# Kernel tuning notes

Measured on AMD Instinct MI355X. Metric: run time of the kernel, lower is better.

The kernel has to match this reference:

```python
import jax, jax.numpy as jnp
import numpy as np
from jax import lax

K = 3; KK = K * K; S = 1; P = 1; D = 1
BN_EPS = 1e-5


def setup_inputs() -> dict:
    key = jax.random.key(0)
    ks = jax.random.split(key, 4)
    B, C, H, W = 8, 128, 64, 64
    cout = 128
    # xavier-ish scales for conv weights
    def xavier(k, shape):
        fan_in = shape[1] * shape[2] * shape[3]
        fan_out = shape[0] * shape[2] * shape[3]
        limit = np.sqrt(6.0 / (fan_in + fan_out))
        return jax.random.uniform(k, shape, jnp.float32, -limit, limit)
    return {
        "x": jax.random.normal(ks[0], (B, C, H, W), jnp.float32),
        "w_off": xavier(ks[1], (2 * KK, C, K, K)),
        "b_off": jnp.zeros((2 * KK,), jnp.float32),
        "w_mod": xavier(ks[2], (KK, C, K, K)),
        "b_mod": jnp.zeros((KK,), jnp.float32),
        "w_reg": xavier(ks[3], (cout, C, K, K)),
        "b_reg": jnp.zeros((cout,), jnp.float32),
        "gamma": jnp.ones((cout,), jnp.float32),
        "beta": jnp.zeros((cout,), jnp.float32),
    }


def _conv(x, w, b):
    y = lax.conv_general_dilated(x, w, (S, S), [(P, P), (P, P)],
                                 rhs_dilation=(D, D),
                                 dimension_numbers=("NCHW", "OIHW", "NCHW"))
    return y + b[None, :, None, None]


def _deform_conv(x, offset, mask, w_reg, b_reg):
    B, C, H, W = x.shape
    Ho, Wo = offset.shape[2], offset.shape[3]
    # torchvision layout: [B, 2*KK, Ho, Wo], interleaved (dy, dx) per tap
    off = offset.reshape(B, KK, 2, Ho, Wo)
    dy, dx = off[:, :, 0], off[:, :, 1]                      # [B,KK,Ho,Wo]
    ki = jnp.arange(KK) // K
    kj = jnp.arange(KK) % K
    base_y = (jnp.arange(Ho) * S - P)[None, :, None] + (ki * D)[:, None, None]  # [KK,Ho,1]
    base_x = (jnp.arange(Wo) * S - P)[None, None, :] + (kj * D)[:, None, None]  # [KK,1,Wo]
    py = base_y[None].astype(x.dtype) + dy                   # [B,KK,Ho,Wo]
    px = base_x[None].astype(x.dtype) + dx

    y0f = jnp.floor(py); x0f = jnp.floor(px)
    ly = py - y0f; lx = px - x0f
    y0 = y0f.astype(jnp.int32); x0 = x0f.astype(jnp.int32)
    y1 = y0 + 1; x1 = x0 + 1

    def gather(iy, ix):
        valid = ((iy >= 0) & (iy < H) & (ix >= 0) & (ix < W)).astype(x.dtype)
        iyc = jnp.clip(iy, 0, H - 1)
        ixc = jnp.clip(ix, 0, W - 1)
        v = jax.vmap(lambda img, a, b: img[:, a, b])(x, iyc, ixc)  # [B,C,KK,Ho,Wo]
        return v * valid[:, None]

    val = (gather(y0, x0) * ((1 - ly) * (1 - lx))[:, None]
           + gather(y0, x1) * ((1 - ly) * lx)[:, None]
           + gather(y1, x0) * (ly * (1 - lx))[:, None]
           + gather(y1, x1) * (ly * lx)[:, None])               # [B,C,KK,Ho,Wo]

    patches = val * mask[:, None]                               # modulated samples
    wr = w_reg.reshape(w_reg.shape[0], C, KK)
    out = jnp.einsum("ock,bckhw->bohw", wr, patches)
    return out + b_reg[None, :, None, None]


def reference(x, w_off, b_off, w_mod, b_mod, w_reg, b_reg, gamma, beta):
    offset = _conv(x, w_off, b_off)
    modulator = 2.0 * jax.nn.sigmoid(_conv(x, w_mod, b_mod))
    y = _deform_conv(x, offset, modulator, w_reg, b_reg)
    # BatchNorm2d (training-mode batch statistics) + ReLU
    mu = y.mean(axis=(0, 2, 3), keepdims=True)
    var = y.var(axis=(0, 2, 3), keepdims=True)
    y = (y - mu) * lax.rsqrt(var + BN_EPS)
    y = y * gamma[None, :, None, None] + beta[None, :, None, None]
    return jax.nn.relu(y)
```

## Files before the change

kernel.cpp:

```cpp
#include <hip/hip_runtime.h>
#include <math.h>

#define H 64
#define W 64
#define C 128
#define NB 8
#define COUT 128
#define HWi 4096
#define NKC 36
#define PADu 40

typedef __attribute__((ext_vector_type(8))) short short8;
typedef __attribute__((ext_vector_type(8))) unsigned short ushort8;
typedef __attribute__((ext_vector_type(4))) unsigned int uint4v;
typedef __attribute__((ext_vector_type(4))) float f32x4;

__device__ __forceinline__ unsigned short f2bf(float f){
    unsigned u = __float_as_uint(f);
    unsigned r = (u + 0x7FFFu + ((u >> 16) & 1u)) >> 16;
    return (unsigned short)r;
}
__device__ __forceinline__ float bf2f(unsigned short u){
    return __uint_as_float(((unsigned)u) << 16);
}
__device__ __forceinline__ unsigned cvtpk_bf16(float lo, float hi){
    unsigned r;
    asm("v_cvt_pk_bf16_f32 %0, %1, %2" : "=v"(r) : "v"(lo), "v"(hi));
    return r;
}

__global__ void k_pre(const float* __restrict__ x, unsigned short* __restrict__ xTp,
                      const float* __restrict__ w_reg, const float* __restrict__ w_off,
                      const float* __restrict__ w_mod, const float* __restrict__ b_off,
                      const float* __restrict__ b_mod,
                      unsigned short* __restrict__ wAv, unsigned short* __restrict__ w27A,
                      float* __restrict__ biasom, float* __restrict__ psum){
    int tid = threadIdx.x;
    if (blockIdx.x >= 528){
        int i = (blockIdx.x - 528) * 256 + tid;
        if (i < 147456){
            int kc = i >> 12, rem = i & 4095;
            int q = rem >> 10, r = (rem >> 3) & 127, j = rem & 7;
            int kk = kc * 32 + q * 8 + j, k = kk >> 7, c = kk & 127;
            wAv[i] = f2bf(w_reg[r * 1152 + c * 9 + k]);
        } else if (i < 147456 + 36864){
            int j2 = i - 147456;
            int kc = j2 >> 10, rem = j2 & 1023;
            int q = rem >> 8, m = (rem >> 3) & 31, t = rem & 7;
            int kkl = q * 8 + t;
            int kk = kc * 32 + kkl, k = kk >> 7, c = kk & 127;
            float v = 0.f;
            if (m < 18) v = w_off[m * 1152 + c * 9 + k];
            else if (m < 27) v = w_mod[(m - 18) * 1152 + c * 9 + k];
            w27A[j2] = f2bf(v);
        } else if (i < 147456 + 36864 + 32){
            int m = i - 147456 - 36864;
            biasom[m] = (m < 18) ? b_off[m] : (m < 27 ? b_mod[m - 18] : 0.f);
        } else if (i < 147456 + 36864 + 32 + 256){
            psum[i - 147456 - 36864 - 32] = 0.f;
        }
        return;
    }
    int bidx = blockIdx.x;
    int b = bidx & 7, hp = bidx >> 3;
    unsigned short* row = xTp + (size_t)(b * 66 + hp) * 66 * 128;
    if (hp == 0 || hp == 65){
        ushort8 z = {0,0,0,0,0,0,0,0};
        for (int i = tid; i < 66 * 128 / 8; i += 256) ((ushort8*)row)[i] = z;
        return;
    }
    int h = hp - 1;
    __shared__ unsigned short s[64 * 136];
    #pragma unroll
    for (int it = 0; it < 8; it++){
        int idx = it * 256 + tid;
        int c = idx >> 4, w4 = (idx & 15) * 4;
        float4 v = *(const float4*)(x + (size_t)(b * 128 + c) * HWi + h * 64 + w4);
        s[(w4 + 0) * 136 + c] = f2bf(v.x);
        s[(w4 + 1) * 136 + c] = f2bf(v.y);
        s[(w4 + 2) * 136 + c] = f2bf(v.z);
        s[(w4 + 3) * 136 + c] = f2bf(v.w);
    }
    __syncthreads();
    if (tid < 32){
        ushort8 z = {0,0,0,0,0,0,0,0};
        int wp = (tid < 16) ? 0 : 65;
        int sg = tid & 15;
        *(ushort8*)(row + wp * 128 + sg * 8) = z;
    }
    for (int it = tid; it < 1024; it += 256){
        int w2 = it >> 4, sg = it & 15;
        *(ushort8*)(row + (w2 + 1) * 128 + sg * 8) = *(const ushort8*)(s + w2 * 136 + sg * 8);
    }
}

__global__ __launch_bounds__(512, 4) void k_fused(const unsigned short* __restrict__ xTp,
        const unsigned short* __restrict__ w27A, const float* __restrict__ biasom,
        const unsigned short* __restrict__ wAv, const float* __restrict__ b_reg,
        unsigned short* __restrict__ ybf, float* __restrict__ psum){
    __shared__ char smem[38912];
    int tid = threadIdx.x;
    int lb = (blockIdx.x & 7) * 64 + (blockIdx.x >> 3);
    int n0 = lb * 64;
    int b = n0 >> 12, h = (n0 >> 6) & 63;

    {
        int grp = tid >> 8, gt = tid & 255;
        unsigned short* pB = (unsigned short*)(smem + grp * 10240);
        int wvg = gt >> 6, lane = gt & 63, quad = lane >> 4, l16 = lane & 15;
        int nl = gt >> 2, sg = gt & 3;
        f32x4 acc0 = {0.f,0.f,0.f,0.f}, acc1 = {0.f,0.f,0.f,0.f};
        int kc0 = grp * 18;
        auto p1load = [&](int i, ushort8& B8){
            int kc = kc0 + i;
            int k = kc >> 2, cb = (kc & 3) << 5;
            int ki = k / 3, kj = k - ki * 3;
            int rowi = (b * 66 + h + ki) * 66 + (nl + kj);
            B8 = *(const ushort8*)(xTp + (size_t)rowi * 128 + cb + sg * 8);
        };
        auto p1body = [&](int i, ushort8& B8){
            int p = i & 1;
            int kc = kc0 + i;
            const unsigned short* wj = w27A + kc * 1024 + quad * 256;
            short8 a0 = *(const short8*)(wj + l16 * 8);
            short8 a1 = *(const short8*)(wj + (16 + l16) * 8);
            *(ushort8*)(pB + p * 2560 + nl * PADu + sg * 8) = B8;
            if (i + 2 < 18) p1load(i + 2, B8);
            __syncthreads();
            short8 bfrag = *(const short8*)(pB + p * 2560 + (wvg * 16 + l16) * PADu + quad * 8);
            acc0 = __builtin_amdgcn_mfma_f32_16x16x32_bf16(a0, bfrag, acc0, 0, 0, 0);
            acc1 = __builtin_amdgcn_mfma_f32_16x16x32_bf16(a1, bfrag, acc1, 0, 0, 0);
        };
        ushort8 rB0, rB1;
        p1load(0, rB0);
        p1load(1, rB1);
        for (int ih = 0; ih < 9; ih++){
            p1body(ih * 2,     rB0);
            p1body(ih * 2 + 1, rB1);
        }
        float* s_red = (float*)(smem + 20480);
        int npx = wvg * 16 + l16;
        if (grp == 1){
            #pragma unroll
            for (int t = 0; t < 2; t++){
                f32x4 a = t ? acc1 : acc0;
                #pragma unroll
                for (int r = 0; r < 4; r++)
                    s_red[npx * 32 + t * 16 + quad * 4 + r] = a[r];
            }
        }
        __syncthreads();
        if (grp == 0){
            unsigned short* s_OM = (unsigned short*)smem;
            #pragma unroll
            for (int t = 0; t < 2; t++){
                f32x4 a = t ? acc1 : acc0;
                #pragma unroll
                for (int r = 0; r < 4; r++){
                    int oc = t * 16 + quad * 4 + r;
                    float v = a[r] + s_red[npx * 32 + oc] + biasom[oc];
                    if (oc >= 18) v = 2.f / (1.f + expf(-v));
                    s_OM[npx * 32 + oc] = f2bf(v);
                }
            }
        }
        __syncthreads();
    }

    unsigned short* sB = (unsigned short*)smem;
    int*   s_a0 = (int*)(smem + 20480);
    float* s_w0 = (float*)(smem + 29696);
    const unsigned short* s_OM = (const unsigned short*)smem;

    for (int idx = tid; idx < 576; idx += 512){
        int k = idx >> 6, px_ = idx & 63;
        float dy = bf2f(s_OM[px_ * 32 + 2 * k]);
        float dx = bf2f(s_OM[px_ * 32 + 2 * k + 1]);
        float m  = bf2f(s_OM[px_ * 32 + 18 + k]);
        int ki = k / 3, kj = k - ki * 3;
        float py  = (float)(h - 1 + ki) + dy;
        float pxf = (float)(px_ - 1 + kj) + dx;
        float y0f = floorf(py), x0f = floorf(pxf);
        float ly = py - y0f, lx = pxf - x0f;
        int iy0 = (int)y0f, ix0 = (int)x0f;
        int cy0 = min(max(iy0 + 1, 0), 65), cy1 = min(max(iy0 + 2, 0), 65);
        int cx0 = min(max(ix0 + 1, 0), 65), cx1 = min(max(ix0 + 2, 0), 65);
        int rb = b * 66 * 66;
        s_a0[0 * 576 + idx] = ((rb + cy0 * 66) + cx0) * 128;
        s_a0[1 * 576 + idx] = ((rb + cy0 * 66) + cx1) * 128;
        s_a0[2 * 576 + idx] = ((rb + cy1 * 66) + cx0) * 128;
        s_a0[3 * 576 + idx] = ((rb + cy1 * 66) + cx1) * 128;
        s_w0[0 * 576 + idx] = (1.f - ly) * (1.f - lx) * m;
        s_w0[1 * 576 + idx] = (1.f - ly) * lx * m;
        s_w0[2 * 576 + idx] = ly * (1.f - lx) * m;
        s_w0[3 * 576 + idx] = ly * lx * m;
    }
    __syncthreads();

    int wv = tid >> 6, lane = tid & 63, quad = lane >> 4, l16 = lane & 15;
    int ocq = wv & 3, ng = wv >> 2;
    int px = tid >> 3, cg2 = tid & 7;

    int rowA0 = ocq * 32 + l16, rowA1 = rowA0 + 16;
    int offB0 = (ng * 32 + l16) * PADu + quad * 8;
    int offB1 = (ng * 32 + 16 + l16) * PADu + quad * 8;

    f32x4 acc00 = {0.f,0.f,0.f,0.f}, acc01 = {0.f,0.f,0.f,0.f};
    f32x4 acc10 = {0.f,0.f,0.f,0.f}, acc11 = {0.f,0.f,0.f,0.f};

    auto loadP = [&](int j, ushort8& C0, ushort8& C1, ushort8& C2, ushort8& C3, float4& Wt){
        int k = j >> 1, cb = (j & 1) << 6;
        int idx = k * 64 + px;
        int co = cb + cg2 * 8;
        Wt.x = s_w0[0 * 576 + idx]; Wt.y = s_w0[1 * 576 + idx];
        Wt.z = s_w0[2 * 576 + idx]; Wt.w = s_w0[3 * 576 + idx];
        C0 = *(const ushort8*)(xTp + s_a0[0 * 576 + idx] + co);
        C1 = *(const ushort8*)(xTp + s_a0[1 * 576 + idx] + co);
        C2 = *(const ushort8*)(xTp + s_a0[2 * 576 + idx] + co);
        C3 = *(const ushort8*)(xTp + s_a0[3 * 576 + idx] + co);
    };
    auto bodyP = [&](int j, ushort8& C0, ushort8& C1, ushort8& C2, ushort8& C3, float4& Wt){
        int p = j & 1;
        unsigned short* sBp = sB + p * 5120;
        const unsigned short* wj = wAv + (size_t)(2 * j) * 4096 + quad * 1024;
        short8 a00 = *(const short8*)(wj + rowA0 * 8);
        short8 a01 = *(const short8*)(wj + rowA1 * 8);
        short8 a10 = *(const short8*)(wj + 4096 + rowA0 * 8);
        short8 a11 = *(const short8*)(wj + 4096 + rowA1 * 8);
        uint4v ov;
        #pragma unroll
        for (int q = 0; q < 4; q++){
            float v0 = Wt.x * bf2f(C0[2*q])   + Wt.y * bf2f(C1[2*q])
                     + Wt.z * bf2f(C2[2*q])   + Wt.w * bf2f(C3[2*q]);
            float v1 = Wt.x * bf2f(C0[2*q+1]) + Wt.y * bf2f(C1[2*q+1])
                     + Wt.z * bf2f(C2[2*q+1]) + Wt.w * bf2f(C3[2*q+1]);
            ov[q] = cvtpk_bf16(v0, v1);
        }
        *(uint4v*)(sBp + (cg2 >> 2) * 2560 + px * PADu + (cg2 & 3) * 8) = ov;
        if (j + 2 < 18) loadP(j + 2, C0, C1, C2, C3, Wt);
        __syncthreads();
        short8 b0 = *(const short8*)(sBp + offB0);
        short8 b1 = *(const short8*)(sBp + offB1);
        acc00 = __builtin_amdgcn_mfma_f32_16x16x32_bf16(a00, b0, acc00, 0, 0, 0);
        acc01 = __builtin_amdgcn_mfma_f32_16x16x32_bf16(a00, b1, acc01, 0, 0, 0);
        acc10 = __builtin_amdgcn_mfma_f32_16x16x32_bf16(a01, b0, acc10, 0, 0, 0);
        acc11 = __builtin_amdgcn_mfma_f32_16x16x32_bf16(a01, b1, acc11, 0, 0, 0);
        b0 = *(const short8*)(sBp + 2560 + offB0);
        b1 = *(const short8*)(sBp + 2560 + offB1);
        acc00 = __builtin_amdgcn_mfma_f32_16x16x32_bf16(a10, b0, acc00, 0, 0, 0);
        acc01 = __builtin_amdgcn_mfma_f32_16x16x32_bf16(a10, b1, acc01, 0, 0, 0);
        acc10 = __builtin_amdgcn_mfma_f32_16x16x32_bf16(a11, b0, acc10, 0, 0, 0);
        acc11 = __builtin_amdgcn_mfma_f32_16x16x32_bf16(a11, b1, acc11, 0, 0, 0);
    };

    ushort8 C0a, C1a, C2a, C3a, C0b, C1b, C2b, C3b;
    float4 Wta, Wtb;
    loadP(0, C0a, C1a, C2a, C3a, Wta);
    loadP(1, C0b, C1b, C2b, C3b, Wtb);
    for (int jh = 0; jh < 9; jh++){
        bodyP(jh * 2,     C0a, C1a, C2a, C3a, Wta);
        bodyP(jh * 2 + 1, C0b, C1b, C2b, C3b, Wtb);
    }

    __syncthreads();
    float* ls = (float*)smem;
    int sp0 = h * 64;
    #pragma unroll
    for (int to = 0; to < 2; to++){
        #pragma unroll
        for (int tn = 0; tn < 2; tn++){
            f32x4 a = to ? (tn ? acc11 : acc10) : (tn ? acc01 : acc00);
            int nl = ng * 32 + tn * 16 + l16;
            #pragma unroll
            for (int r = 0; r < 4; r++){
                int oc = ocq * 32 + to * 16 + quad * 4 + r;
                float v = a[r] + b_reg[oc];
                ybf[(size_t)(b * 128 + oc) * HWi + sp0 + nl] = f2bf(v);
                ls[oc * 67 + nl] = v;
            }
        }
    }
    __syncthreads();
    if (tid < 128){
        int oc = tid;
        float s = 0.f, s2 = 0.f;
        #pragma unroll 8
        for (int nl = 0; nl < 64; nl++){
            float v = ls[oc * 67 + nl];
            s += v; s2 = fmaf(v, v, s2);
        }
        atomicAdd(&psum[oc], s);
        atomicAdd(&psum[128 + oc], s2);
    }
}

__global__ void k_apply(const unsigned short* __restrict__ ybf, const float* __restrict__ psum,
                        const float* __restrict__ gamma, const float* __restrict__ beta,
                        float* __restrict__ out){
    int lb = ((int)blockIdx.x & 7) * 256 + ((int)blockIdx.x >> 3);
    int e8 = (lb * 256 + (int)threadIdx.x) * 8;
    int c = (e8 >> 12) & 127;
    ushort8 u = *(const ushort8*)(ybf + e8);
    float s = psum[c], s2 = psum[128 + c];
    float mean = s * (1.f / 32768.f);
    float var  = s2 * (1.f / 32768.f) - mean * mean;
    float rs = rsqrtf(var + 1e-5f);
    float g = gamma[c] * rs;
    float bt = beta[c] - mean * g;
    float4 lo, hi;
    lo.x = fmaxf(fmaf(bf2f(u[0]), g, bt), 0.f);
    lo.y = fmaxf(fmaf(bf2f(u[1]), g, bt), 0.f);
    lo.z = fmaxf(fmaf(bf2f(u[2]), g, bt), 0.f);
    lo.w = fmaxf(fmaf(bf2f(u[3]), g, bt), 0.f);
    hi.x = fmaxf(fmaf(bf2f(u[4]), g, bt), 0.f);
    hi.y = fmaxf(fmaf(bf2f(u[5]), g, bt), 0.f);
    hi.z = fmaxf(fmaf(bf2f(u[6]), g, bt), 0.f);
    hi.w = fmaxf(fmaf(bf2f(u[7]), g, bt), 0.f);
    *(float4*)(out + e8)     = lo;
    *(float4*)(out + e8 + 4) = hi;
}

extern "C" void kernel_launch(void* const* d_in, const int* in_sizes, int n_in,
                              void* d_out, int out_size, void* d_ws, size_t ws_size,
                              hipStream_t stream){
    const float* x     = (const float*)d_in[0];
    const float* w_off = (const float*)d_in[1];
    const float* b_off = (const float*)d_in[2];
    const float* w_mod = (const float*)d_in[3];
    const float* b_mod = (const float*)d_in[4];
    const float* w_reg = (const float*)d_in[5];
    const float* b_reg = (const float*)d_in[6];
    const float* gamma = (const float*)d_in[7];
    const float* beta  = (const float*)d_in[8];

    char* wsb = (char*)d_ws;
    unsigned short* xTp   = (unsigned short*)(wsb);
    unsigned short* ybf   = (unsigned short*)(wsb + 11018240);
    unsigned short* wAv   = (unsigned short*)(wsb + 19406848);
    unsigned short* w27A  = (unsigned short*)(wsb + 19701760);
    float*          biasom= (float*)(wsb + 19775488);
    float*          psum  = (float*)(wsb + 19775616);
    float* out = (float*)d_out;

    hipLaunchKernelGGL(k_pre,   dim3(1250), dim3(256), 0, stream, x, xTp, w_reg, w_off, w_mod, b_off, b_mod, wAv, w27A, biasom, psum);
    hipLaunchKernelGGL(k_fused, dim3(512),  dim3(512), 0, stream, xTp, w27A, biasom, wAv, b_reg, ybf, psum);
    hipLaunchKernelGGL(k_apply, dim3(2048), dim3(256), 0, stream, ybf, psum, gamma, beta, out);
}
```

Baseline: 132.1 us.

## Halve fused-kernel pixel tile to 32 and use 256-thread blocks

```diff
diff --git a/kernel.cpp b/kernel.cpp
--- a/kernel.cpp
+++ b/kernel.cpp
@@ -94,134 +94,115 @@
     }
 }
 
-__global__ __launch_bounds__(512, 4) void k_fused(const unsigned short* __restrict__ xTp,
+__global__ __launch_bounds__(256, 4) void k_fused(const unsigned short* __restrict__ xTp,
         const unsigned short* __restrict__ w27A, const float* __restrict__ biasom,
         const unsigned short* __restrict__ wAv, const float* __restrict__ b_reg,
         unsigned short* __restrict__ ybf, float* __restrict__ psum){
-    __shared__ char smem[38912];
+    __shared__ char smem[21504];
     int tid = threadIdx.x;
-    int lb = (blockIdx.x & 7) * 64 + (blockIdx.x >> 3);
-    int n0 = lb * 64;
-    int b = n0 >> 12, h = (n0 >> 6) & 63;
+    int lb = (blockIdx.x & 7) * 128 + (blockIdx.x >> 3);
+    int n0 = lb * 32;
+    int b = n0 >> 12, h = (n0 >> 6) & 63, w0 = n0 & 63;
+
+    int wv = tid >> 6, lane = tid & 63, quad = lane >> 4, l16 = lane & 15;
 
     {
-        int grp = tid >> 8, gt = tid & 255;
-        unsigned short* pB = (unsigned short*)(smem + grp * 10240);
-        int wvg = gt >> 6, lane = gt & 63, quad = lane >> 4, l16 = lane & 15;
-        int nl = gt >> 2, sg = gt & 3;
-        f32x4 acc0 = {0.f,0.f,0.f,0.f}, acc1 = {0.f,0.f,0.f,0.f};
-        int kc0 = grp * 18;
-        auto p1load = [&](int i, ushort8& B8){
-            int kc = kc0 + i;
+        unsigned short* pB = (unsigned short*)smem;
+        int mt = wv >> 1, nt = wv & 1;
+        int pl = tid >> 7, spx = (tid >> 2) & 31, sg = tid & 3;
+        f32x4 acc = {0.f,0.f,0.f,0.f};
+        auto p1load = [&](int j, ushort8& B8){
+            int kc = 2 * j + pl;
             int k = kc >> 2, cb = (kc & 3) << 5;
             int ki = k / 3, kj = k - ki * 3;
-            int rowi = (b * 66 + h + ki) * 66 + (nl + kj);
+            int rowi = (b * 66 + h + ki) * 66 + (w0 + spx + kj);
             B8 = *(const ushort8*)(xTp + (size_t)rowi * 128 + cb + sg * 8);
         };
-        auto p1body = [&](int i, ushort8& B8){
-            int p = i & 1;
-            int kc = kc0 + i;
-            const unsigned short* wj = w27A + kc * 1024 + quad * 256;
-            short8 a0 = *(const short8*)(wj + l16 * 8);
-            short8 a1 = *(const short8*)(wj + (16 + l16) * 8);
-            *(ushort8*)(pB + p * 2560 + nl * PADu + sg * 8) = B8;
-            if (i + 2 < 18) p1load(i + 2, B8);
+        auto p1body = [&](int j, ushort8& B8){
+            int p = j & 1;
+            unsigned short* pBp = pB + p * 2560;
+            const unsigned short* wj0 = w27A + (2 * j) * 1024 + quad * 256;
+            const unsigned short* wj1 = w27A + (2 * j + 1) * 1024 + quad * 256;
+            short8 a0 = *(const short8*)(wj0 + (mt * 16 + l16) * 8);
+            short8 a1 = *(const short8*)(wj1 + (mt * 16 + l16) * 8);
+            *(ushort8*)(pBp + pl * 1280 + spx * PADu + sg * 8) = B8;
+            if (j + 2 < 18) p1load(j + 2, B8);
             __syncthreads();
-            short8 bfrag = *(const short8*)(pB + p * 2560 + (wvg * 16 + l16) * PADu + quad * 8);
-            acc0 = __builtin_amdgcn_mfma_f32_16x16x32_bf16(a0, bfrag, acc0, 0, 0, 0);
-            acc1 = __builtin_amdgcn_mfma_f32_16x16x32_bf16(a1, bfrag, acc1, 0, 0, 0);
+            short8 b0 = *(const short8*)(pBp + (nt * 16 + l16) * PADu + quad * 8);
+            short8 b1 = *(const short8*)(pBp + 1280 + (nt * 16 + l16) * PADu + quad * 8);
+            acc = __builtin_amdgcn_mfma_f32_16x16x32_bf16(a0, b0, acc, 0, 0, 0);
+            acc = __builtin_amdgcn_mfma_f32_16x16x32_bf16(a1, b1, acc, 0, 0, 0);
         };
         ushort8 rB0, rB1;
         p1load(0, rB0);
         p1load(1, rB1);
-        for (int ih = 0; ih < 9; ih++){
-            p1body(ih * 2,     rB0);
-            p1body(ih * 2 + 1, rB1);
-        }
-        float* s_red = (float*)(smem + 20480);
-        int npx = wvg * 16 + l16;
-        if (grp == 1){
-            #pragma unroll
-            for (int t = 0; t < 2; t++){
-                f32x4 a = t ? acc1 : acc0;
-                #pragma unroll
-                for (int r = 0; r < 4; r++)
-                    s_red[npx * 32 + t * 16 + quad * 4 + r] = a[r];
-            }
+        for (int jh = 0; jh < 9; jh++){
+            p1body(jh * 2,     rB0);
+            p1body(jh * 2 + 1, rB1);
+        }
+        unsigned short* s_OM = (unsigned short*)(smem + 10240);
+        #pragma unroll
+        for (int r = 0; r < 4; r++){
+            int oc = mt * 16 + quad * 4 + r;
+            float v = acc[r] + biasom[oc];
+            if (oc >= 18) v = 2.f / (1.f + expf(-v));
+            s_OM[(nt * 16 + l16) * 32 + oc] = f2bf(v);
         }
         __syncthreads();
-        if (grp == 0){
-            unsigned short* s_OM = (unsigned short*)smem;
-            #pragma unroll
-            for (int t = 0; t < 2; t++){
-                f32x4 a = t ? acc1 : acc0;
-                #pragma unroll
-                for (int r = 0; r < 4; r++){
-                    int oc = t * 16 + quad * 4 + r;
-                    float v = a[r] + s_red[npx * 32 + oc] + biasom[oc];
-                    if (oc >= 18) v = 2.f / (1.f + expf(-v));
-                    s_OM[npx * 32 + oc] = f2bf(v);
-                }
-            }
-        }
-        __syncthreads();
     }
 
     unsigned short* sB = (unsigned short*)smem;
-    int*   s_a0 = (int*)(smem + 20480);
-    float* s_w0 = (float*)(smem + 29696);
-    const unsigned short* s_OM = (const unsigned short*)smem;
-
-    for (int idx = tid; idx < 576; idx += 512){
-        int k = idx >> 6, px_ = idx & 63;
+    int*   s_a0 = (int*)(smem + 12288);
+    float* s_w0 = (float*)(smem + 16896);
+    const unsigned short* s_OM = (const unsigned short*)(smem + 10240);
+
+    for (int idx = tid; idx < 288; idx += 256){
+        int k = idx >> 5, px_ = idx & 31;
         float dy = bf2f(s_OM[px_ * 32 + 2 * k]);
         float dx = bf2f(s_OM[px_ * 32 + 2 * k + 1]);
         float m  = bf2f(s_OM[px_ * 32 + 18 + k]);
         int ki = k / 3, kj = k - ki * 3;
         float py  = (float)(h - 1 + ki) + dy;
-        float pxf = (float)(px_ - 1 + kj) + dx;
+        float pxf = (float)(w0 + px_ - 1 + kj) + dx;
         float y0f = floorf(py), x0f = floorf(pxf);
         float ly = py - y0f, lx = pxf - x0f;
         int iy0 = (int)y0f, ix0 = (int)x0f;
         int cy0 = min(max(iy0 + 1, 0), 65), cy1 = min(max(iy0 + 2, 0), 65);
         int cx0 = min(max(ix0 + 1, 0), 65), cx1 = min(max(ix0 + 2, 0), 65);
         int rb = b * 66 * 66;
-        s_a0[0 * 576 + idx] = ((rb + cy0 * 66) + cx0) * 128;
-        s_a0[1 * 576 + idx] = ((rb + cy0 * 66) + cx1) * 128;
-        s_a0[2 * 576 + idx] = ((rb + cy1 * 66) + cx0) * 128;
-        s_a0[3 * 576 + idx] = ((rb + cy1 * 66) + cx1) * 128;
-        s_w0[0 * 576 + idx] = (1.f - ly) * (1.f - lx) * m;
-        s_w0[1 * 576 + idx] = (1.f - ly) * lx * m;
-        s_w0[2 * 576 + idx] = ly * (1.f - lx) * m;
-        s_w0[3 * 576 + idx] = ly * lx * m;
+        s_a0[0 * 288 + idx] = ((rb + cy0 * 66) + cx0) * 128;
+        s_a0[1 * 288 + idx] = ((rb + cy0 * 66) + cx1) * 128;
+        s_a0[2 * 288 + idx] = ((rb + cy1 * 66) + cx0) * 128;
+        s_a0[3 * 288 + idx] = ((rb + cy1 * 66) + cx1) * 128;
+        s_w0[0 * 288 + idx] = (1.f - ly) * (1.f - lx) * m;
+        s_w0[1 * 288 + idx] = (1.f - ly) * lx * m;
+        s_w0[2 * 288 + idx] = ly * (1.f - lx) * m;
+        s_w0[3 * 288 + idx] = ly * lx * m;
     }
     __syncthreads();
 
-    int wv = tid >> 6, lane = tid & 63, quad = lane >> 4, l16 = lane & 15;
-    int ocq = wv & 3, ng = wv >> 2;
     int px = tid >> 3, cg2 = tid & 7;
-
-    int rowA0 = ocq * 32 + l16, rowA1 = rowA0 + 16;
-    int offB0 = (ng * 32 + l16) * PADu + quad * 8;
-    int offB1 = (ng * 32 + 16 + l16) * PADu + quad * 8;
+    int rowA0 = wv * 32 + l16, rowA1 = rowA0 + 16;
+    int offB0 = l16 * PADu + quad * 8;
+    int offB1 = (16 + l16) * PADu + quad * 8;
 
     f32x4 acc00 = {0.f,0.f,0.f,0.f}, acc01 = {0.f,0.f,0.f,0.f};
     f32x4 acc10 = {0.f,0.f,0.f,0.f}, acc11 = {0.f,0.f,0.f,0.f};
 
     auto loadP = [&](int j, ushort8& C0, ushort8& C1, ushort8& C2, ushort8& C3, float4& Wt){
         int k = j >> 1, cb = (j & 1) << 6;
-        int idx = k * 64 + px;
+        int idx = k * 32 + px;
         int co = cb + cg2 * 8;
-        Wt.x = s_w0[0 * 576 + idx]; Wt.y = s_w0[1 * 576 + idx];
-        Wt.z = s_w0[2 * 576 + idx]; Wt.w = s_w0[3 * 576 + idx];
-        C0 = *(const ushort8*)(xTp + s_a0[0 * 576 + idx] + co);
-        C1 = *(const ushort8*)(xTp + s_a0[1 * 576 + idx] + co);
-        C2 = *(const ushort8*)(xTp + s_a0[2 * 576 + idx] + co);
-        C3 = *(const ushort8*)(xTp + s_a0[3 * 576 + idx] + co);
+        Wt.x = s_w0[0 * 288 + idx]; Wt.y = s_w0[1 * 288 + idx];
+        Wt.z = s_w0[2 * 288 + idx]; Wt.w = s_w0[3 * 288 + idx];
+        C0 = *(const ushort8*)(xTp + s_a0[0 * 288 + idx] + co);
+        C1 = *(const ushort8*)(xTp + s_a0[1 * 288 + idx] + co);
+        C2 = *(const ushort8*)(xTp + s_a0[2 * 288 + idx] + co);
+        C3 = *(const ushort8*)(xTp + s_a0[3 * 288 + idx] + co);
     };
     auto bodyP = [&](int j, ushort8& C0, ushort8& C1, ushort8& C2, ushort8& C3, float4& Wt){
         int p = j & 1;
-        unsigned short* sBp = sB + p * 5120;
+        unsigned short* sBp = sB + p * 2560;
         const unsigned short* wj = wAv + (size_t)(2 * j) * 4096 + quad * 1024;
         short8 a00 = *(const short8*)(wj + rowA0 * 8);
         short8 a01 = *(const short8*)(wj + rowA1 * 8);
@@ -236,7 +217,7 @@
                      + Wt.z * bf2f(C2[2*q+1]) + Wt.w * bf2f(C3[2*q+1]);
             ov[q] = cvtpk_bf16(v0, v1);
         }
-        *(uint4v*)(sBp + (cg2 >> 2) * 2560 + px * PADu + (cg2 & 3) * 8) = ov;
+        *(uint4v*)(sBp + (cg2 >> 2) * 1280 + px * PADu + (cg2 & 3) * 8) = ov;
         if (j + 2 < 18) loadP(j + 2, C0, C1, C2, C3, Wt);
         __syncthreads();
         short8 b0 = *(const short8*)(sBp + offB0);
@@ -245,8 +226,8 @@
         acc01 = __builtin_amdgcn_mfma_f32_16x16x32_bf16(a00, b1, acc01, 0, 0, 0);
         acc10 = __builtin_amdgcn_mfma_f32_16x16x32_bf16(a01, b0, acc10, 0, 0, 0);
         acc11 = __builtin_amdgcn_mfma_f32_16x16x32_bf16(a01, b1, acc11, 0, 0, 0);
-        b0 = *(const short8*)(sBp + 2560 + offB0);
-        b1 = *(const short8*)(sBp + 2560 + offB1);
+        b0 = *(const short8*)(sBp + 1280 + offB0);
+        b1 = *(const short8*)(sBp + 1280 + offB1);
         acc00 = __builtin_amdgcn_mfma_f32_16x16x32_bf16(a10, b0, acc00, 0, 0, 0);
         acc01 = __builtin_amdgcn_mfma_f32_16x16x32_bf16(a10, b1, acc01, 0, 0, 0);
         acc10 = __builtin_amdgcn_mfma_f32_16x16x32_bf16(a11, b0, acc10, 0, 0, 0);
@@ -264,19 +245,19 @@
 
     __syncthreads();
     float* ls = (float*)smem;
-    int sp0 = h * 64;
+    int sp0 = h * 64 + w0;
     #pragma unroll
-    for (int to = 0; to < 2; to++){
+    for (int mt = 0; mt < 2; mt++){
         #pragma unroll
-        for (int tn = 0; tn < 2; tn++){
-            f32x4 a = to ? (tn ? acc11 : acc10) : (tn ? acc01 : acc00);
-            int nl = ng * 32 + tn * 16 + l16;
+        for (int nt = 0; nt < 2; nt++){
+            f32x4 a = mt ? (nt ? acc11 : acc10) : (nt ? acc01 : acc00);
+            int pxl = nt * 16 + l16;
             #pragma unroll
             for (int r = 0; r < 4; r++){
-                int oc = ocq * 32 + to * 16 + quad * 4 + r;
+                int oc = wv * 32 + mt * 16 + quad * 4 + r;
                 float v = a[r] + b_reg[oc];
-                ybf[(size_t)(b * 128 + oc) * HWi + sp0 + nl] = f2bf(v);
-                ls[oc * 67 + nl] = v;
+                ybf[(size_t)(b * 128 + oc) * HWi + sp0 + pxl] = f2bf(v);
+                ls[oc * 33 + pxl] = v;
             }
         }
     }
@@ -285,8 +266,8 @@
         int oc = tid;
         float s = 0.f, s2 = 0.f;
         #pragma unroll 8
-        for (int nl = 0; nl < 64; nl++){
-            float v = ls[oc * 67 + nl];
+        for (int pxl = 0; pxl < 32; pxl++){
+            float v = ls[oc * 33 + pxl];
             s += v; s2 = fmaf(v, v, s2);
         }
         atomicAdd(&psum[oc], s);
@@ -343,6 +324,6 @@
     float* out = (float*)d_out;
 
     hipLaunchKernelGGL(k_pre,   dim3(1250), dim3(256), 0, stream, x, xTp, w_reg, w_off, w_mod, b_off, b_mod, wAv, w27A, biasom, psum);
-    hipLaunchKernelGGL(k_fused, dim3(512),  dim3(512), 0, stream, xTp, w27A, biasom, wAv, b_reg, ybf, psum);
+    hipLaunchKernelGGL(k_fused, dim3(1024), dim3(256), 0, stream, xTp, w27A, biasom, wAv, b_reg, ybf, psum);
     hipLaunchKernelGGL(k_apply, dim3(2048), dim3(256), 0, stream, ybf, psum, gamma, beta, out);
 }
```

Result: slower. 138.6 us (+4.9%).
